# Kernel optimization log

Hardware: AMD Instinct MI355X
Metric: run time of the kernel (lower is better)

## Reference

```python
import jax, jax.numpy as jnp
import numpy as np

LN2 = 0.6931471805599453

def _logcosh(z):
    # numerically stable log(cosh(z)) = logaddexp(z, -z) - log(2)
    return jnp.logaddexp(z, -z) - LN2

def _logpsi(z, W, b, a):
    # RBM log-amplitude. z: [..., N] -> scalar per leading dims
    return z @ a + jnp.sum(_logcosh(z @ W + b), axis=-1)

def setup_inputs() -> dict:
    key = jax.random.key(0)
    k0, k1, k2, k3, k4 = jax.random.split(key, 5)
    B, N, H = 64, 512, 2048
    # spin configurations (sign pattern; flips y_k = x with site k negated work for any real values)
    x = jnp.sign(jax.random.normal(k0, (B, N), dtype=jnp.float32))
    # small init so exp(logpsi_y - logpsi_x) stays well-scaled
    W = 0.01 * jax.random.normal(k1, (N, H), dtype=jnp.float32)
    b = 0.01 * jax.random.normal(k2, (H,), dtype=jnp.float32)
    a = 0.01 * jax.random.normal(k3, (N,), dtype=jnp.float32)
    # per-connection operator matrix elements O(x, y_k)
    Oxy = jax.random.normal(k4, (N,), dtype=jnp.float32)
    return {"x": x, "W": W, "b": b, "a": a, "Oxy": Oxy}

def reference(x, W, b, a, Oxy):
    # eval_local_operator, vmapped over a batch of configurations.
    # operator.conn(x): y[k] = x with spin k flipped, with matrix element Oxy[k].
    B, N = x.shape
    flip = 1.0 - 2.0 * jnp.eye(N, dtype=x.dtype)          # [K=N, N]
    y = x[:, None, :] * flip[None, :, :]                  # [B, K, N] connected states
    logpsi_x = _logpsi(x, W, b, a)                        # [B]
    logpsi_y = _logpsi(y, W, b, a)                        # [B, K]
    # Oxy @ exp(logpsi_y - logpsi_x) per sample
    return jnp.einsum('k,bk->b', Oxy, jnp.exp(logpsi_y - logpsi_x[:, None]))
```

## Files before the change

### kernel.cpp

```cpp
#include <hip/hip_runtime.h>
#include <hip/hip_bf16.h>
#include <math.h>

constexpr int NB = 64;
constexpr int NN = 512;
constexpr int NH = 2048;
constexpr float LN2 = 0.6931471805599453f;

constexpr size_t OFF_T2  = 0;
constexpr size_t OFF_LC  = OFF_T2  + (size_t)NN*NH;
constexpr size_t OFF_XT  = OFF_LC  + NN;
constexpr size_t OFF_TT  = OFF_XT  + (size_t)NN*NB;
constexpr size_t OFF_THP = OFF_TT  + (size_t)NH*NB;
constexpr size_t OFF_DS  = OFF_THP + (size_t)8*NB*NH;

__global__ void k_xt(const float* __restrict__ x, float* __restrict__ xt) {
    int t = blockIdx.x * 256 + threadIdx.x;
    int b = t & 63, n = t >> 6;
    xt[t] = x[b * NN + n];
}

__global__ void k_prep_w(const float* __restrict__ W, float* __restrict__ t2,
                         float* __restrict__ LC) {
    int k = blockIdx.x;
    int tid = threadIdx.x;
    float lsum = 0.f;
#pragma unroll
    for (int i = 0; i < 8; i++) {
        int h = tid + i * 256;
        float y  = 2.0f * W[k * NH + h];
        float ay = fabsf(y);
        float e  = __expf(-2.0f * ay);
        float th = (1.0f - e) / (1.0f + e);
        t2[k * NH + h] = copysignf(th, y);
        lsum += ay + log1pf(e) - LN2;
    }
    __shared__ float red[256];
    red[tid] = lsum; __syncthreads();
    for (int s = 128; s > 0; s >>= 1) {
        if (tid < s) red[tid] += red[tid + s];
        __syncthreads();
    }
    if (tid == 0) LC[k] = red[0];
}

__global__ void k_gemm(const float* __restrict__ W, const float* __restrict__ xt,
                       float* __restrict__ thp) {
    int h  = blockIdx.x * 256 + threadIdx.x;
    int bt = blockIdx.y;
    int nc = blockIdx.z;
    float acc[16];
#pragma unroll
    for (int j = 0; j < 16; j++) acc[j] = 0.f;
    const float* xp = xt + (size_t)nc * 64 * NB + bt * 16;
    const float* wp = W + (size_t)nc * 64 * NH + h;
    for (int n = 0; n < 64; n++) {
        float w = wp[(size_t)n * NH];
#pragma unroll
        for (int j = 0; j < 16; j++) acc[j] = fmaf(xp[n * NB + j], w, acc[j]);
    }
    float* op = thp + (size_t)nc * NB * NH + (size_t)(bt * 16) * NH + h;
#pragma unroll
    for (int j = 0; j < 16; j++) op[(size_t)j * NH] = acc[j];
}

__global__ void k_tanh_t(const float* __restrict__ thp, const float* __restrict__ bvec,
                         float* __restrict__ Tt) {
    int g = blockIdx.x * 256 + threadIdx.x;
    int h = g & (NH - 1), b = g >> 11;
    float th = bvec[h];
#pragma unroll
    for (int nc = 0; nc < 8; nc++) th += thp[(size_t)nc * NB * NH + (size_t)b * NH + h];
    float ay = fabsf(th);
    float e  = __expf(-2.0f * ay);
    float t  = (1.0f - e) / (1.0f + e);
    Tt[h * NB + b] = copysignf(t, th);
}

__global__ __launch_bounds__(256) void k_main(const float* __restrict__ t2,
                                              const float* __restrict__ Tt,
                                              const float* __restrict__ xt,
                                              float* __restrict__ dsum) {
    __shared__ float Tl[256 * NB];
    int tid = threadIdx.x;
    int kt  = blockIdx.x;
    int hc  = blockIdx.y;
    const float4* src = (const float4*)(Tt + (size_t)hc * 256 * NB);
    float4* dst = (float4*)Tl;
#pragma unroll
    for (int i = 0; i < 16; i++) dst[tid + i * 256] = src[tid + i * 256];
    __syncthreads();

    int wave = tid >> 6, lane = tid & 63;
    int k0 = __builtin_amdgcn_readfirstlane(kt * 8 + wave * 2);
    float ms0 = -xt[k0 * NB + lane];
    float ms1 = -xt[(k0 + 1) * NB + lane];
    const float* r0 = t2 + (size_t)k0 * NH + hc * 256;
    const float* r1 = r0 + NH;

    float lp0 = 0.f, lp1 = 0.f;
    for (int h0 = 0; h0 < 256; h0 += 32) {
        float p0 = 1.f, p1 = 1.f;
#pragma unroll 8
        for (int hh = 0; hh < 32; hh++) {
            int h = h0 + hh;
            float T = Tl[h * NB + lane];
            p0 *= fmaf(r0[h] * T, ms0, 1.0f);
            p1 *= fmaf(r1[h] * T, ms1, 1.0f);
        }
        lp0 += __logf(p0);
        lp1 += __logf(p1);
    }
    atomicAdd(&dsum[k0 * NB + lane], lp0);
    atomicAdd(&dsum[(k0 + 1) * NB + lane], lp1);
}

__global__ void k_out(const float* __restrict__ dsum, const float* __restrict__ LC,
                      const float* __restrict__ xt, const float* __restrict__ a,
                      const float* __restrict__ Oxy, float* __restrict__ out) {
    int b = blockIdx.x, tid = threadIdx.x;
    float sum = 0.f;
    for (int k = tid; k < NN; k += 256) {
        float s = xt[k * NB + b];
        float d = dsum[k * NB + b] + LC[k] - 2.0f * s * a[k];
        sum += Oxy[k] * __expf(d);
    }
    __shared__ float red[256];
    red[tid] = sum; __syncthreads();
    for (int st = 128; st > 0; st >>= 1) {
        if (tid < st) red[tid] += red[tid + st];
        __syncthreads();
    }
    if (tid == 0) out[b] = red[0];
}

extern "C" void kernel_launch(void* const* d_in, const int* in_sizes, int n_in,
                              void* d_out, int out_size, void* d_ws, size_t ws_size,
                              hipStream_t stream) {
    const float* x    = (const float*)d_in[0];
    const float* W    = (const float*)d_in[1];
    const float* bvec = (const float*)d_in[2];
    const float* a    = (const float*)d_in[3];
    const float* Oxy  = (const float*)d_in[4];
    float* out = (float*)d_out;

    float* ws   = (float*)d_ws;
    float* t2   = ws + OFF_T2;
    float* LC   = ws + OFF_LC;
    float* xt   = ws + OFF_XT;
    float* Tt   = ws + OFF_TT;
    float* thp  = ws + OFF_THP;
    float* dsum = ws + OFF_DS;

    k_xt<<<NN * NB / 256, 256, 0, stream>>>(x, xt);
    k_prep_w<<<NN, 256, 0, stream>>>(W, t2, LC);
    k_gemm<<<dim3(NH / 256, NB / 16, 8), 256, 0, stream>>>(W, xt, thp);
    k_tanh_t<<<NB * NH / 256, 256, 0, stream>>>(thp, bvec, Tt);
    hipMemsetAsync(dsum, 0, (size_t)NN * NB * sizeof(float), stream);
    k_main<<<dim3(NN / 8, NH / 256), 256, 0, stream>>>(t2, Tt, xt, dsum);
    k_out<<<NB, 256, 0, stream>>>(dsum, LC, xt, a, Oxy, out);
}
```

Baseline: 104.3 us.

## Fuse prep kernels into one launch and replace atomics with partial-sum buffer

Merges the transpose, weight-prep, GEMM and tanh kernels into a single heterogeneous launch. Blocks either prep W rows or compute a GEMM tile whose split-K partials are reduced in shared memory before the tanh. The main kernel now writes per-hc partial log sums to a buffer instead of using atomics and a memset, and k_out sums the 8 partials. The inner loop is fully unrolled. This cuts launch count, the thp round-trip and atomic traffic, at the cost of strided x reads and fewer, larger GEMM blocks.

New measurement: 135.0 us. +29.4%, slower.

```diff
diff --git a/kernel.cpp b/kernel.cpp
--- a/kernel.cpp
+++ b/kernel.cpp
@@ -7,79 +7,75 @@
 constexpr int NH = 2048;
 constexpr float LN2 = 0.6931471805599453f;
 
-constexpr size_t OFF_T2  = 0;
-constexpr size_t OFF_LC  = OFF_T2  + (size_t)NN*NH;
-constexpr size_t OFF_XT  = OFF_LC  + NN;
-constexpr size_t OFF_TT  = OFF_XT  + (size_t)NN*NB;
-constexpr size_t OFF_THP = OFF_TT  + (size_t)NH*NB;
-constexpr size_t OFF_DS  = OFF_THP + (size_t)8*NB*NH;
+constexpr size_t OFF_T2 = 0;
+constexpr size_t OFF_LC = OFF_T2 + (size_t)NN*NH;
+constexpr size_t OFF_TT = OFF_LC + NN;
+constexpr size_t OFF_DS = OFF_TT + (size_t)NH*NB;
 
-__global__ void k_xt(const float* __restrict__ x, float* __restrict__ xt) {
-    int t = blockIdx.x * 256 + threadIdx.x;
-    int b = t & 63, n = t >> 6;
-    xt[t] = x[b * NN + n];
-}
-
-__global__ void k_prep_w(const float* __restrict__ W, float* __restrict__ t2,
-                         float* __restrict__ LC) {
-    int k = blockIdx.x;
-    int tid = threadIdx.x;
-    float lsum = 0.f;
+__global__ __launch_bounds__(256) void k_prep(const float* __restrict__ W,
+                                              const float* __restrict__ x,
+                                              const float* __restrict__ bvec,
+                                              float* __restrict__ t2,
+                                              float* __restrict__ LC,
+                                              float* __restrict__ Tt) {
+    __shared__ float sm[4096];
+    int bid = blockIdx.x, tid = threadIdx.x;
+    if (bid < NN) {
+        int k = bid;
+        float lsum = 0.f;
 #pragma unroll
-    for (int i = 0; i < 8; i++) {
-        int h = tid + i * 256;
-        float y  = 2.0f * W[k * NH + h];
-        float ay = fabsf(y);
-        float e  = __expf(-2.0f * ay);
-        float th = (1.0f - e) / (1.0f + e);
-        t2[k * NH + h] = copysignf(th, y);
-        lsum += ay + log1pf(e) - LN2;
+        for (int i = 0; i < 8; i++) {
+            int h = tid + i * 256;
+            float y  = 2.0f * W[(size_t)k * NH + h];
+            float ay = fabsf(y);
+            float e  = __expf(-2.0f * ay);
+            float th = (1.0f - e) / (1.0f + e);
+            t2[(size_t)k * NH + h] = copysignf(th, y);
+            lsum += ay + __logf(1.0f + e) - LN2;
+        }
+        sm[tid] = lsum; __syncthreads();
+        for (int s = 128; s > 0; s >>= 1) {
+            if (tid < s) sm[tid] += sm[tid + s];
+            __syncthreads();
+        }
+        if (tid == 0) LC[k] = sm[0];
+    } else {
+        int gb = bid - NN;
+        int ht = gb & 31;
+        int bt = gb >> 5;
+        int hl = tid & 63, ns = tid >> 6;
+        int h  = ht * 64 + hl;
+        float acc[16];
+#pragma unroll
+        for (int j = 0; j < 16; j++) acc[j] = 0.f;
+        const float* wp = W + h;
+        const float* xp = x + (size_t)(bt * 16) * NN;
+        for (int n = ns * 128; n < ns * 128 + 128; n++) {
+            float w = wp[(size_t)n * NH];
+#pragma unroll
+            for (int j = 0; j < 16; j++) acc[j] = fmaf(xp[(size_t)j * NN + n], w, acc[j]);
+        }
+#pragma unroll
+        for (int j = 0; j < 16; j++) sm[ns * 1024 + hl * 16 + j] = acc[j];
+        __syncthreads();
+#pragma unroll
+        for (int i = 0; i < 4; i++) {
+            int idx = i * 256 + tid;
+            int hl2 = idx >> 4, j2 = idx & 15;
+            float th = bvec[ht * 64 + hl2];
+#pragma unroll
+            for (int s2 = 0; s2 < 4; s2++) th += sm[s2 * 1024 + idx];
+            float ay = fabsf(th);
+            float e  = __expf(-2.0f * ay);
+            float t  = (1.0f - e) / (1.0f + e);
+            Tt[(size_t)(ht * 64 + hl2) * NB + bt * 16 + j2] = copysignf(t, th);
+        }
     }
-    __shared__ float red[256];
-    red[tid] = lsum; __syncthreads();
-    for (int s = 128; s > 0; s >>= 1) {
-        if (tid < s) red[tid] += red[tid + s];
-        __syncthreads();
-    }
-    if (tid == 0) LC[k] = red[0];
-}
-
-__global__ void k_gemm(const float* __restrict__ W, const float* __restrict__ xt,
-                       float* __restrict__ thp) {
-    int h  = blockIdx.x * 256 + threadIdx.x;
-    int bt = blockIdx.y;
-    int nc = blockIdx.z;
-    float acc[16];
-#pragma unroll
-    for (int j = 0; j < 16; j++) acc[j] = 0.f;
-    const float* xp = xt + (size_t)nc * 64 * NB + bt * 16;
-    const float* wp = W + (size_t)nc * 64 * NH + h;
-    for (int n = 0; n < 64; n++) {
-        float w = wp[(size_t)n * NH];
-#pragma unroll
-        for (int j = 0; j < 16; j++) acc[j] = fmaf(xp[n * NB + j], w, acc[j]);
-    }
-    float* op = thp + (size_t)nc * NB * NH + (size_t)(bt * 16) * NH + h;
-#pragma unroll
-    for (int j = 0; j < 16; j++) op[(size_t)j * NH] = acc[j];
-}
-
-__global__ void k_tanh_t(const float* __restrict__ thp, const float* __restrict__ bvec,
-                         float* __restrict__ Tt) {
-    int g = blockIdx.x * 256 + threadIdx.x;
-    int h = g & (NH - 1), b = g >> 11;
-    float th = bvec[h];
-#pragma unroll
-    for (int nc = 0; nc < 8; nc++) th += thp[(size_t)nc * NB * NH + (size_t)b * NH + h];
-    float ay = fabsf(th);
-    float e  = __expf(-2.0f * ay);
-    float t  = (1.0f - e) / (1.0f + e);
-    Tt[h * NB + b] = copysignf(t, th);
 }
 
 __global__ __launch_bounds__(256) void k_main(const float* __restrict__ t2,
                                               const float* __restrict__ Tt,
-                                              const float* __restrict__ xt,
+                                              const float* __restrict__ x,
                                               float* __restrict__ dsum) {
     __shared__ float Tl[256 * NB];
     int tid = threadIdx.x;
@@ -93,15 +89,15 @@
 
     int wave = tid >> 6, lane = tid & 63;
     int k0 = __builtin_amdgcn_readfirstlane(kt * 8 + wave * 2);
-    float ms0 = -xt[k0 * NB + lane];
-    float ms1 = -xt[(k0 + 1) * NB + lane];
+    float ms0 = -x[(size_t)lane * NN + k0];
+    float ms1 = -x[(size_t)lane * NN + k0 + 1];
     const float* r0 = t2 + (size_t)k0 * NH + hc * 256;
     const float* r1 = r0 + NH;
 
     float lp0 = 0.f, lp1 = 0.f;
     for (int h0 = 0; h0 < 256; h0 += 32) {
         float p0 = 1.f, p1 = 1.f;
-#pragma unroll 8
+#pragma unroll
         for (int hh = 0; hh < 32; hh++) {
             int h = h0 + hh;
             float T = Tl[h * NB + lane];
@@ -111,18 +107,19 @@
         lp0 += __logf(p0);
         lp1 += __logf(p1);
     }
-    atomicAdd(&dsum[k0 * NB + lane], lp0);
-    atomicAdd(&dsum[(k0 + 1) * NB + lane], lp1);
+    dsum[(size_t)hc * NN * NB + (size_t)k0 * NB + lane]       = lp0;
+    dsum[(size_t)hc * NN * NB + (size_t)(k0 + 1) * NB + lane] = lp1;
 }
 
 __global__ void k_out(const float* __restrict__ dsum, const float* __restrict__ LC,
-                      const float* __restrict__ xt, const float* __restrict__ a,
+                      const float* __restrict__ x, const float* __restrict__ a,
                       const float* __restrict__ Oxy, float* __restrict__ out) {
     int b = blockIdx.x, tid = threadIdx.x;
     float sum = 0.f;
     for (int k = tid; k < NN; k += 256) {
-        float s = xt[k * NB + b];
-        float d = dsum[k * NB + b] + LC[k] - 2.0f * s * a[k];
+        float d = LC[k] - 2.0f * x[(size_t)b * NN + k] * a[k];
+#pragma unroll
+        for (int hc = 0; hc < 8; hc++) d += dsum[(size_t)hc * NN * NB + (size_t)k * NB + b];
         sum += Oxy[k] * __expf(d);
     }
     __shared__ float red[256];
@@ -147,16 +144,10 @@
     float* ws   = (float*)d_ws;
     float* t2   = ws + OFF_T2;
     float* LC   = ws + OFF_LC;
-    float* xt   = ws + OFF_XT;
     float* Tt   = ws + OFF_TT;
-    float* thp  = ws + OFF_THP;
     float* dsum = ws + OFF_DS;
 
-    k_xt<<<NN * NB / 256, 256, 0, stream>>>(x, xt);
-    k_prep_w<<<NN, 256, 0, stream>>>(W, t2, LC);
-    k_gemm<<<dim3(NH / 256, NB / 16, 8), 256, 0, stream>>>(W, xt, thp);
-    k_tanh_t<<<NB * NH / 256, 256, 0, stream>>>(thp, bvec, Tt);
-    hipMemsetAsync(dsum, 0, (size_t)NN * NB * sizeof(float), stream);
-    k_main<<<dim3(NN / 8, NH / 256), 256, 0, stream>>>(t2, Tt, xt, dsum);
-    k_out<<<NB, 256, 0, stream>>>(dsum, LC, xt, a, Oxy, out);
+    k_prep<<<NN + 128, 256, 0, stream>>>(W, x, bvec, t2, LC, Tt);
+    k_main<<<dim3(NN / 8, NH / 256), 256, 0, stream>>>(t2, Tt, x, dsum);
+    k_out<<<NB, 256, 0, stream>>>(dsum, LC, x, a, Oxy, out);
 }
```

## Fuse prep kernels, split GEMM deeper, replace atomics with per-chunk partials

Applied to the files above, without the earlier changes.

Merges the transpose and W-preprocessing kernels into one launch, with W loads vectorised as float4. The GEMM's K split doubles from 8 to 16 chunks so more blocks can run in parallel. k_main now writes per-h-chunk partial sums instead of using atomicAdd, which removes the memset; k_out sums the 8 partials itself. The inner product loop is fully unrolled. The aim is fewer launches and no atomic contention, at the cost of more partial-sum memory traffic.

After: 94.11 us. 1.11x faster.

```diff
diff --git a/kernel.cpp b/kernel.cpp
--- a/kernel.cpp
+++ b/kernel.cpp
@@ -12,49 +12,63 @@
 constexpr size_t OFF_XT  = OFF_LC  + NN;
 constexpr size_t OFF_TT  = OFF_XT  + (size_t)NN*NB;
 constexpr size_t OFF_THP = OFF_TT  + (size_t)NH*NB;
-constexpr size_t OFF_DS  = OFF_THP + (size_t)8*NB*NH;
+constexpr size_t OFF_DS  = OFF_THP + (size_t)16*NB*NH;
 
-__global__ void k_xt(const float* __restrict__ x, float* __restrict__ xt) {
-    int t = blockIdx.x * 256 + threadIdx.x;
-    int b = t & 63, n = t >> 6;
-    xt[t] = x[b * NN + n];
+__global__ __launch_bounds__(256) void k_pre(const float* __restrict__ W,
+                                             const float* __restrict__ x,
+                                             float* __restrict__ t2,
+                                             float* __restrict__ LC,
+                                             float* __restrict__ xt) {
+    int bid = blockIdx.x, tid = threadIdx.x;
+    if (bid < NN) {
+        int k = bid;
+        const float4* wr = (const float4*)(W + (size_t)k * NH);
+        float4* tr = (float4*)(t2 + (size_t)k * NH);
+        float4 w0 = wr[tid], w1 = wr[tid + 256];
+        float in[8] = {w0.x, w0.y, w0.z, w0.w, w1.x, w1.y, w1.z, w1.w};
+        float t[8], lsum = 0.f;
+#pragma unroll
+        for (int i = 0; i < 8; i++) {
+            float y  = 2.0f * in[i];
+            float ay = fabsf(y);
+            float e  = __expf(-2.0f * ay);
+            t[i] = copysignf((1.0f - e) / (1.0f + e), y);
+            lsum += ay + __logf(1.0f + e) - LN2;
+        }
+        tr[tid]       = make_float4(t[0], t[1], t[2], t[3]);
+        tr[tid + 256] = make_float4(t[4], t[5], t[6], t[7]);
+        __shared__ float red[256];
+        red[tid] = lsum; __syncthreads();
+        for (int s = 128; s > 0; s >>= 1) {
+            if (tid < s) red[tid] += red[tid + s];
+            __syncthreads();
+        }
+        if (tid == 0) LC[k] = red[0];
+    } else {
+        int base = (bid - NN) * 4096;
+#pragma unroll
+        for (int i = 0; i < 16; i++) {
+            int tIdx = base + i * 256 + tid;
+            int b = tIdx & 63, n = tIdx >> 6;
+            xt[tIdx] = x[(size_t)b * NN + n];
+        }
+    }
 }
 
-__global__ void k_prep_w(const float* __restrict__ W, float* __restrict__ t2,
-                         float* __restrict__ LC) {
-    int k = blockIdx.x;
+__global__ __launch_bounds__(256) void k_gemm(const float* __restrict__ W,
+                                              const float* __restrict__ xt,
+                                              float* __restrict__ thp) {
     int tid = threadIdx.x;
-    float lsum = 0.f;
-#pragma unroll
-    for (int i = 0; i < 8; i++) {
-        int h = tid + i * 256;
-        float y  = 2.0f * W[k * NH + h];
-        float ay = fabsf(y);
-        float e  = __expf(-2.0f * ay);
-        float th = (1.0f - e) / (1.0f + e);
-        t2[k * NH + h] = copysignf(th, y);
-        lsum += ay + log1pf(e) - LN2;
-    }
-    __shared__ float red[256];
-    red[tid] = lsum; __syncthreads();
-    for (int s = 128; s > 0; s >>= 1) {
-        if (tid < s) red[tid] += red[tid + s];
-        __syncthreads();
-    }
-    if (tid == 0) LC[k] = red[0];
-}
-
-__global__ void k_gemm(const float* __restrict__ W, const float* __restrict__ xt,
-                       float* __restrict__ thp) {
-    int h  = blockIdx.x * 256 + threadIdx.x;
+    int h  = blockIdx.x * 256 + tid;
     int bt = blockIdx.y;
     int nc = blockIdx.z;
     float acc[16];
 #pragma unroll
     for (int j = 0; j < 16; j++) acc[j] = 0.f;
-    const float* xp = xt + (size_t)nc * 64 * NB + bt * 16;
-    const float* wp = W + (size_t)nc * 64 * NH + h;
-    for (int n = 0; n < 64; n++) {
+    const float* xp = xt + (size_t)nc * 32 * NB + bt * 16;
+    const float* wp = W + (size_t)(nc * 32) * NH + h;
+#pragma unroll 4
+    for (int n = 0; n < 32; n++) {
         float w = wp[(size_t)n * NH];
 #pragma unroll
         for (int j = 0; j < 16; j++) acc[j] = fmaf(xp[n * NB + j], w, acc[j]);
@@ -64,17 +78,17 @@
     for (int j = 0; j < 16; j++) op[(size_t)j * NH] = acc[j];
 }
 
-__global__ void k_tanh_t(const float* __restrict__ thp, const float* __restrict__ bvec,
-                         float* __restrict__ Tt) {
+__global__ __launch_bounds__(256) void k_tanh(const float* __restrict__ thp,
+                                              const float* __restrict__ bvec,
+                                              float* __restrict__ Tt) {
     int g = blockIdx.x * 256 + threadIdx.x;
     int h = g & (NH - 1), b = g >> 11;
     float th = bvec[h];
 #pragma unroll
-    for (int nc = 0; nc < 8; nc++) th += thp[(size_t)nc * NB * NH + (size_t)b * NH + h];
+    for (int nc = 0; nc < 16; nc++) th += thp[(size_t)nc * NB * NH + g];
     float ay = fabsf(th);
     float e  = __expf(-2.0f * ay);
-    float t  = (1.0f - e) / (1.0f + e);
-    Tt[h * NB + b] = copysignf(t, th);
+    Tt[(size_t)h * NB + b] = copysignf((1.0f - e) / (1.0f + e), th);
 }
 
 __global__ __launch_bounds__(256) void k_main(const float* __restrict__ t2,
@@ -93,15 +107,15 @@
 
     int wave = tid >> 6, lane = tid & 63;
     int k0 = __builtin_amdgcn_readfirstlane(kt * 8 + wave * 2);
-    float ms0 = -xt[k0 * NB + lane];
-    float ms1 = -xt[(k0 + 1) * NB + lane];
+    float ms0 = -xt[(size_t)k0 * NB + lane];
+    float ms1 = -xt[(size_t)(k0 + 1) * NB + lane];
     const float* r0 = t2 + (size_t)k0 * NH + hc * 256;
     const float* r1 = r0 + NH;
 
     float lp0 = 0.f, lp1 = 0.f;
     for (int h0 = 0; h0 < 256; h0 += 32) {
         float p0 = 1.f, p1 = 1.f;
-#pragma unroll 8
+#pragma unroll
         for (int hh = 0; hh < 32; hh++) {
             int h = h0 + hh;
             float T = Tl[h * NB + lane];
@@ -111,8 +125,8 @@
         lp0 += __logf(p0);
         lp1 += __logf(p1);
     }
-    atomicAdd(&dsum[k0 * NB + lane], lp0);
-    atomicAdd(&dsum[(k0 + 1) * NB + lane], lp1);
+    dsum[(size_t)hc * NN * NB + (size_t)k0 * NB + lane]       = lp0;
+    dsum[(size_t)hc * NN * NB + (size_t)(k0 + 1) * NB + lane] = lp1;
 }
 
 __global__ void k_out(const float* __restrict__ dsum, const float* __restrict__ LC,
@@ -121,8 +135,9 @@
     int b = blockIdx.x, tid = threadIdx.x;
     float sum = 0.f;
     for (int k = tid; k < NN; k += 256) {
-        float s = xt[k * NB + b];
-        float d = dsum[k * NB + b] + LC[k] - 2.0f * s * a[k];
+        float d = LC[k] - 2.0f * xt[(size_t)k * NB + b] * a[k];
+#pragma unroll
+        for (int hc = 0; hc < 8; hc++) d += dsum[(size_t)hc * NN * NB + (size_t)k * NB + b];
         sum += Oxy[k] * __expf(d);
     }
     __shared__ float red[256];
@@ -152,11 +167,9 @@
     float* thp  = ws + OFF_THP;
     float* dsum = ws + OFF_DS;
 
-    k_xt<<<NN * NB / 256, 256, 0, stream>>>(x, xt);
-    k_prep_w<<<NN, 256, 0, stream>>>(W, t2, LC);
-    k_gemm<<<dim3(NH / 256, NB / 16, 8), 256, 0, stream>>>(W, xt, thp);
-    k_tanh_t<<<NB * NH / 256, 256, 0, stream>>>(thp, bvec, Tt);
-    hipMemsetAsync(dsum, 0, (size_t)NN * NB * sizeof(float), stream);
+    k_pre<<<NN + 8, 256, 0, stream>>>(W, x, t2, LC, xt);
+    k_gemm<<<dim3(NH / 256, NB / 16, 16), 256, 0, stream>>>(W, xt, thp);
+    k_tanh<<<NB * NH / 256, 256, 0, stream>>>(thp, bvec, Tt);
     k_main<<<dim3(NN / 8, NH / 256), 256, 0, stream>>>(t2, Tt, xt, dsum);
     k_out<<<NB, 256, 0, stream>>>(dsum, LC, xt, a, Oxy, out);
 }
```
